# Kernel optimization log

Hardware: AMD Instinct MI355X
Metric: run time of the kernel (lower is better)

Reference implementation:

```python
import jax, jax.numpy as jnp
from jax import lax
import numpy as np

BETA = 0.5
ITERATION = 50
K = 1
EPS = 1e-5  # F.normalize eps


def cost_matrix_cosine(x, y):
    # x: [b,m,d], y: [b,n,d] -> cosine distance [b,m,n]
    xn = x / jnp.maximum(jnp.linalg.norm(x, axis=-1, keepdims=True), EPS)
    yn = y / jnp.maximum(jnp.linalg.norm(y, axis=-1, keepdims=True), EPS)
    return 1.0 - jnp.einsum('bmd,bnd->bmn', xn, yn)


def ipot(C, x_len, x_pad, y_len, y_pad, joint_pad, beta, iteration, k):
    # C: [b,m,n]; x_*: txt (m); y_*: img (n). Returns transport plan [b,m,n].
    b, m, n = C.shape
    jp_t = jnp.transpose(joint_pad, (0, 2, 1))                      # [b,n,m]
    A = jnp.where(jp_t, 0.0, jnp.exp(-jnp.transpose(C, (0, 2, 1)) / beta))
    T0 = jnp.where(jp_t, 0.0, 1.0)                                  # [b,n,m]
    sigma0 = jnp.where(x_pad, 0.0, 1.0 / x_len[:, None])[:, :, None]  # [b,m,1]
    x_mask = (x_pad.astype(C.dtype) * 1e4)[:, None, :]              # [b,1,m]
    y_mask = (y_pad.astype(C.dtype) * 1e4)[:, None, :]              # [b,1,n]
    xl = x_len[:, None, None]
    yl = y_len[:, None, None]

    def outer(carry, _):
        T, sigma = carry
        Q = A * T                                                   # [b,n,m]
        def inner(sig, _):
            # sig: [b,m,1]
            delta = 1.0 / (yl * jnp.transpose(jnp.matmul(Q, sig), (0, 2, 1)) + y_mask)  # [b,1,n]
            sig = jnp.transpose(1.0 / (xl * jnp.matmul(delta, Q) + x_mask), (0, 2, 1))  # [b,m,1]
            return sig, delta
        sigma, deltas = lax.scan(inner, sigma, None, length=k)
        delta = deltas[-1]                                          # [b,1,n]
        T = jnp.transpose(delta, (0, 2, 1)) * Q * jnp.transpose(sigma, (0, 2, 1))  # [b,n,m]
        return (T, sigma), None

    (T, _), _ = lax.scan(outer, (T0, sigma0), None, length=iteration)
    return jnp.transpose(T, (0, 2, 1))                              # [b,m,n]


def optimal_transport_dist(txt_emb, img_emb, txt_pad, img_pad):
    cost = cost_matrix_cosine(txt_emb, img_emb)                     # [b,m,n]
    joint_pad = txt_pad[:, :, None] | img_pad[:, None, :]           # [b,m,n]
    cost = jnp.where(joint_pad, 0.0, cost)
    txt_len = (txt_pad.shape[1] - jnp.sum(txt_pad, axis=1)).astype(cost.dtype)
    img_len = (img_pad.shape[1] - jnp.sum(img_pad, axis=1)).astype(cost.dtype)
    T = ipot(lax.stop_gradient(cost), txt_len, txt_pad, img_len, img_pad,
             joint_pad, BETA, ITERATION, K)
    # trace(cost @ T^T) == sum_ij cost_ij * plan_ij, per sample
    return jnp.sum(cost * lax.stop_gradient(T), axis=(1, 2))        # [b]


def reference(entitytxt_vec, object_vec, entitytxt_num, object_num):
    txt_nodes_emb = entitytxt_vec.astype(jnp.float32)               # [b,tl,d]
    img_nodes_emb = object_vec[:, 1:].astype(jnp.float32)           # [b,il,d]
    txt_pad = entitytxt_num == 0                                    # [b,tl] bool
    img_pad = object_num[:, 1:] == 0                                # [b,il] bool
    ot_dist = optimal_transport_dist(txt_nodes_emb, img_nodes_emb, txt_pad, img_pad)
    ot_loss = jnp.sum(ot_dist) * 0.01
    return ot_loss


def setup_inputs():
    key = jax.random.key(0)
    k1, k2, k3, k4 = jax.random.split(key, 4)
    b, tl, il1, d = 256, 128, 128, 1024
    entitytxt_vec = jax.random.normal(k1, (b, tl, d), dtype=jnp.float32)
    object_vec = jax.random.normal(k2, (b, il1, d), dtype=jnp.float32)
    entitytxt_num = jax.random.randint(k3, (b, tl), 0, 2, dtype=jnp.int32)
    object_num = jax.random.randint(k4, (b, il1), 0, 2, dtype=jnp.int32)
    # guarantee at least one valid node per sample (avoid 1/0 lengths)
    entitytxt_num = entitytxt_num.at[:, 0].set(1)
    object_num = object_num.at[:, 1].set(1)
    return {"entitytxt_vec": entitytxt_vec, "object_vec": object_vec,
            "entitytxt_num": entitytxt_num, "object_num": object_num}
```

## Files before the change

### kernel.cpp

```cpp
#include <hip/hip_runtime.h>
#include <math.h>

#define BATCH 256
#define M 128
#define NIMG 127
#define NP 128
#define D 1024
#define BK 64
#define NT (D / BK)
#define ITERS 50
#define LROW 72

typedef __attribute__((ext_vector_type(8))) short bf16x8;
typedef __attribute__((ext_vector_type(4))) float floatx4;

static __device__ __forceinline__ unsigned pack_bf16x2(float a, float b) {
    unsigned ua = __builtin_bit_cast(unsigned, a);
    unsigned ub = __builtin_bit_cast(unsigned, b);
    ua += 0x7fffu + ((ua >> 16) & 1u);
    ub += 0x7fffu + ((ub >> 16) & 1u);
    return (ua >> 16) | (ub & 0xffff0000u);
}

template<int CTRL>
static __device__ __forceinline__ float dpp_add(float v) {
    int s = __builtin_amdgcn_update_dpp(0, __builtin_bit_cast(int, v), CTRL, 0xf, 0xf, true);
    return v + __builtin_bit_cast(float, s);
}
static __device__ __forceinline__ float red16(float v) {
    v = dpp_add<0x121>(v);
    v = dpp_add<0x122>(v);
    v = dpp_add<0x124>(v);
    v = dpp_add<0x128>(v);
    return v;
}

static __device__ __forceinline__ void barrier_lgkm() {
    asm volatile("s_waitcnt lgkmcnt(0)" ::: "memory");
    __builtin_amdgcn_s_barrier();
    __builtin_amdgcn_sched_barrier(0);
}

static __device__ __forceinline__ void load_tile(const float* __restrict__ xb,
                                                 const float* __restrict__ yb,
                                                 int kk, int r0, int c16,
                                                 float4 (&vx)[4], float4 (&vy)[4]) {
#pragma unroll
    for (int it = 0; it < 4; ++it) {
        const int r = r0 + it * 32;
        vx[it] = *(const float4*)(xb + (size_t)r * D + kk + c16 * 4);
        float4 z = make_float4(0.f, 0.f, 0.f, 0.f);
        if (r < NIMG) z = *(const float4*)(yb + (size_t)r * D + kk + c16 * 4);
        vy[it] = z;
    }
}

static __device__ __forceinline__ void stage_tile(short* __restrict__ Xs, short* __restrict__ Ys,
                                                  int r0, int c16,
                                                  const float4 (&vx)[4], const float4 (&vy)[4],
                                                  float (&ssx)[4], float (&ssy)[4]) {
#pragma unroll
    for (int it = 0; it < 4; ++it) {
        const int r = r0 + it * 32;
        float4 v = vx[it];
        ssx[it] = fmaf(v.x, v.x, fmaf(v.y, v.y, fmaf(v.z, v.z, fmaf(v.w, v.w, ssx[it]))));
        uint2 p;
        p.x = pack_bf16x2(v.x, v.y);
        p.y = pack_bf16x2(v.z, v.w);
        *(uint2*)(&Xs[r * LROW + c16 * 4]) = p;
        v = vy[it];
        ssy[it] = fmaf(v.x, v.x, fmaf(v.y, v.y, fmaf(v.z, v.z, fmaf(v.w, v.w, ssy[it]))));
        p.x = pack_bf16x2(v.x, v.y);
        p.y = pack_bf16x2(v.z, v.w);
        *(uint2*)(&Ys[r * LROW + c16 * 4]) = p;
    }
}

static __device__ __forceinline__ void mfma_tile(const short* __restrict__ Xs,
                                                 const short* __restrict__ Ys,
                                                 int mbase, int nbase, int col, int quad,
                                                 floatx4 (&acc)[2][4]) {
#pragma unroll
    for (int ks = 0; ks < 2; ++ks) {
        const int koff = ks * 32 + quad * 8;
        bf16x8 af[2], bfr[4];
#pragma unroll
        for (int tr = 0; tr < 2; ++tr)
            af[tr] = *(const bf16x8*)(&Xs[(mbase + tr * 16 + col) * LROW + koff]);
#pragma unroll
        for (int tc = 0; tc < 4; ++tc)
            bfr[tc] = *(const bf16x8*)(&Ys[(nbase + tc * 16 + col) * LROW + koff]);
#pragma unroll
        for (int tr = 0; tr < 2; ++tr)
#pragma unroll
            for (int tc = 0; tc < 4; ++tc)
                acc[tr][tc] = __builtin_amdgcn_mfma_f32_16x16x32_bf16(
                    af[tr], bfr[tc], acc[tr][tc], 0, 0, 0);
    }
}

__launch_bounds__(512, 1)
__global__ void gemm_a_kernel(const float* __restrict__ xg,
                              const float* __restrict__ yg,
                              const int* __restrict__ xnum,
                              const int* __restrict__ ynum,
                              float* __restrict__ Aout)
{
    __shared__ __align__(16) short Xs[2][M * LROW];
    __shared__ __align__(16) short Ys[2][M * LROW];
    __shared__ __align__(16) float sinvx[M];
    __shared__ __align__(16) float sinvy[NP];
    __shared__ __align__(16) float sxmask[M];
    __shared__ __align__(16) float symask[NP];

    const int b    = blockIdx.x;
    const int t    = threadIdx.x;
    const int lane = t & 63;
    const int w    = t >> 6;

    const float* xb = xg + (size_t)b * M * D;
    const float* yb = yg + ((size_t)b * 128 + 1) * D;

    if (t < M)  sxmask[t] = (xnum[b * M + t] == 0) ? 1.0f : 0.0f;
    if (t < NP) symask[t] = (t < NIMG && ynum[b * 128 + t + 1] != 0) ? 0.0f : 1.0f;

    const int r0  = t >> 4;
    const int c16 = t & 15;

    floatx4 acc[2][4];
#pragma unroll
    for (int a = 0; a < 2; ++a)
#pragma unroll
        for (int c = 0; c < 4; ++c) acc[a][c] = (floatx4)0.0f;

    float ssx[4] = {0.f, 0.f, 0.f, 0.f};
    float ssy[4] = {0.f, 0.f, 0.f, 0.f};

    const int mbase = (w & 3) * 32;
    const int nbase = (w >> 2) * 64;
    const int col   = lane & 15;
    const int quad  = lane >> 4;

    float4 vxa[4], vya[4], vxb[4], vyb[4];
    load_tile(xb, yb, 0,  r0, c16, vxa, vya);
    load_tile(xb, yb, BK, r0, c16, vxb, vyb);

#pragma unroll 1
    for (int ii = 0; ii < NT; ii += 2) {
        stage_tile(Xs[0], Ys[0], r0, c16, vxa, vya, ssx, ssy);
        if (ii + 2 < NT) load_tile(xb, yb, (ii + 2) * BK, r0, c16, vxa, vya);
        barrier_lgkm();
        mfma_tile(Xs[0], Ys[0], mbase, nbase, col, quad, acc);
        stage_tile(Xs[1], Ys[1], r0, c16, vxb, vyb, ssx, ssy);
        if (ii + 3 < NT) load_tile(xb, yb, (ii + 3) * BK, r0, c16, vxb, vyb);
        barrier_lgkm();
        mfma_tile(Xs[1], Ys[1], mbase, nbase, col, quad, acc);
    }

#pragma unroll
    for (int it = 0; it < 4; ++it) {
        ssx[it] = red16(ssx[it]);
        ssy[it] = red16(ssy[it]);
    }
    if (c16 == 0) {
#pragma unroll
        for (int it = 0; it < 4; ++it) {
            const int r = r0 + it * 32;
            sinvx[r] = 1.0f / fmaxf(sqrtf(ssx[it]), 1e-5f);
            sinvy[r] = 1.0f / fmaxf(sqrtf(ssy[it]), 1e-5f);
        }
    }
    barrier_lgkm();

    float* Ab = Aout + (size_t)b * M * NP;
#pragma unroll
    for (int tr = 0; tr < 2; ++tr)
#pragma unroll
        for (int tc = 0; tc < 4; ++tc) {
            const int n = nbase + tc * 16 + col;
            const float ivy_n = sinvy[n];
            const float ymf   = symask[n];
#pragma unroll
            for (int reg = 0; reg < 4; ++reg) {
                const int m = mbase + tr * 16 + quad * 4 + reg;
                const float p = acc[tr][tc][reg] * sinvx[m] * ivy_n;
                const float a = (sxmask[m] + ymf > 0.0f) ? 0.0f : expf(2.0f * p - 2.0f);
                Ab[m * NP + n] = a;
            }
        }
}

__launch_bounds__(512, 1)
__global__ void ipot_kernel(const float* __restrict__ Ain,
                            const int* __restrict__ xnum,
                            const int* __restrict__ ynum,
                            float* __restrict__ out)
{
    __shared__ __align__(16) float partCS[8 * 128];
    __shared__ __align__(16) float sdelta[NP];
    __shared__ __align__(16) float sxmask[M];
    __shared__ __align__(16) float symask[NP];
    __shared__ float sxl_s, syl_s;
    __shared__ unsigned scnt[16];
    __shared__ float swsum[8];

    const int b    = blockIdx.x;
    const int t    = threadIdx.x;
    const int lane = t & 63;
    const int w    = t >> 6;
    const int tj   = t & 15;
    const int i0   = (t >> 4) * 4;
    const int j0   = tj * 8;

    bool tpad = true, ipad = true;
    if (t < M)  { tpad = (xnum[b * M + t] == 0); sxmask[t] = tpad ? 1e4f : 0.0f; }
    if (t < NP) { ipad = !(t < NIMG && ynum[b * 128 + t + 1] != 0); symask[t] = ipad ? 1e4f : 0.0f; }
    unsigned long long bx = __ballot(t < M  && !tpad);
    unsigned long long by = __ballot(t < NP && !ipad);
    if (lane == 0) { scnt[w] = (unsigned)__popcll(bx); scnt[8 + w] = (unsigned)__popcll(by); }
    __syncthreads();
    if (t == 0) {
        float xl = 0.f, yl = 0.f;
        for (int k = 0; k < 8; ++k) { xl += scnt[k]; yl += scnt[8 + k]; }
        sxl_s = xl; syl_s = yl;
    }
    __syncthreads();
    const float xl = sxl_s, yl = syl_s;

    float xm[4], ym[8];
    *(float4*)xm       = *(const float4*)(&sxmask[i0]);
    *(float4*)ym       = *(const float4*)(&symask[j0]);
    *(float4*)(ym + 4) = *(const float4*)(&symask[j0 + 4]);

    float sn[4];
#pragma unroll
    for (int r = 0; r < 4; ++r)
        sn[r] = (xm[r] > 0.0f) ? 0.0f : __builtin_amdgcn_rcpf(xl);

    const float* Ab = Ain + (size_t)b * M * NP;
    float Af[4][8], Q[4][8];
#pragma unroll
    for (int r = 0; r < 4; ++r) {
        float4 a0 = *(const float4*)(Ab + (size_t)(i0 + r) * NP + j0);
        float4 a1 = *(const float4*)(Ab + (size_t)(i0 + r) * NP + j0 + 4);
        Af[r][0] = a0.x; Af[r][1] = a0.y; Af[r][2] = a0.z; Af[r][3] = a0.w;
        Af[r][4] = a1.x; Af[r][5] = a1.y; Af[r][6] = a1.z; Af[r][7] = a1.w;
#pragma unroll
        for (int j = 0; j < 8; ++j) Q[r][j] = Af[r][j];
    }

    float lp = 0.0f;
    for (int itn = 0; itn < ITERS; ++itn) {
        float cp[8] = {0.f,0.f,0.f,0.f,0.f,0.f,0.f,0.f};
#pragma unroll
        for (int r = 0; r < 4; ++r)
#pragma unroll
            for (int j = 0; j < 8; ++j)
                cp[j] = fmaf(sn[r], Q[r][j], cp[j]);
#pragma unroll
        for (int j = 0; j < 8; ++j) {
            cp[j] += __shfl_xor(cp[j], 16);
            cp[j] += __shfl_xor(cp[j], 32);
        }
        if (lane < 16) {
            float4 c0 = make_float4(cp[0], cp[1], cp[2], cp[3]);
            float4 c1 = make_float4(cp[4], cp[5], cp[6], cp[7]);
            *(float4*)(&partCS[w * 128 + j0])     = c0;
            *(float4*)(&partCS[w * 128 + j0 + 4]) = c1;
        }
        __syncthreads();
        if (t < NP) {
            float s = 0.f;
#pragma unroll
            for (int w8 = 0; w8 < 8; ++w8) s += partCS[w8 * 128 + t];
            sdelta[t] = __builtin_amdgcn_rcpf(yl * s + symask[t]);
        }
        __syncthreads();
        float dl[8];
        *(float4*)dl       = *(const float4*)(&sdelta[j0]);
        *(float4*)(dl + 4) = *(const float4*)(&sdelta[j0 + 4]);
        float rp[4] = {0.f, 0.f, 0.f, 0.f};
#pragma unroll
        for (int r = 0; r < 4; ++r)
#pragma unroll
            for (int j = 0; j < 8; ++j)
                rp[r] = fmaf(dl[j], Q[r][j], rp[r]);
#pragma unroll
        for (int r = 0; r < 4; ++r) rp[r] = red16(rp[r]);
#pragma unroll
        for (int r = 0; r < 4; ++r) rp[r] = __shfl(rp[r], lane & 48);
#pragma unroll
        for (int r = 0; r < 4; ++r)
            sn[r] = __builtin_amdgcn_rcpf(xl * rp[r] + xm[r]);

        if (itn < ITERS - 1) {
#pragma unroll
            for (int r = 0; r < 4; ++r) {
                const float f = sn[r];
#pragma unroll
                for (int j = 0; j < 8; ++j)
                    Q[r][j] *= Af[r][j] * dl[j] * f;
            }
        } else {
#pragma unroll
            for (int r = 0; r < 4; ++r)
#pragma unroll
                for (int j = 0; j < 8; ++j) {
                    const float a = Af[r][j];
                    if (a > 0.0f)
                        lp = fmaf(-0.5f * logf(a) * dl[j] * sn[r], Q[r][j], lp);
                }
        }
    }

#pragma unroll
    for (int off = 32; off > 0; off >>= 1) lp += __shfl_down(lp, off);
    if (lane == 0) swsum[w] = lp;
    __syncthreads();
    if (t == 0) {
        float tot = 0.f;
        for (int k = 0; k < 8; ++k) tot += swsum[k];
        atomicAdd(out, 0.01f * tot);
    }
}

extern "C" void kernel_launch(void* const* d_in, const int* in_sizes, int n_in,
                              void* d_out, int out_size, void* d_ws, size_t ws_size,
                              hipStream_t stream) {
    const float* x  = (const float*)d_in[0];
    const float* y  = (const float*)d_in[1];
    const int*   xn = (const int*)d_in[2];
    const int*   yn = (const int*)d_in[3];
    float* out = (float*)d_out;
    float* A   = (float*)d_ws;

    (void)hipMemsetAsync(out, 0, (size_t)out_size * sizeof(float), stream);
    gemm_a_kernel<<<dim3(BATCH), dim3(512), 0, stream>>>(x, y, xn, yn, A);
    ipot_kernel<<<dim3(BATCH), dim3(512), 0, stream>>>(A, xn, yn, out);
}
```

Measured before the change: 346.8 us.

## Split cost GEMM over K halves and fuse normalization into IPOT kernel

Adds a GEMM kernel that splits the 1024-long reduction into two halves, launching twice as many blocks (two per batch) with launch bounds allowing two blocks per CU, and writes partial dot products and partial squared norms to workspace. A new IPOT kernel sums the partials, applies the cosine normalization and exp to build A, and keeps the iteration state in registers, updating Q in place. The aim is to fill more CUs during the GEMM phase, since 256 blocks underuse the machine. In exchange it writes and reads back twice as much intermediate data, and it falls back to the old path when the workspace is too small.

```diff
diff --git a/kernel.cpp b/kernel.cpp
--- a/kernel.cpp
+++ b/kernel.cpp
@@ -8,6 +8,8 @@
 #define D 1024
 #define BK 64
 #define NT (D / BK)
+#define KH 512
+#define NT2 (KH / BK)
 #define ITERS 50
 #define LROW 72
 
@@ -99,6 +101,244 @@
     }
 }
 
+__launch_bounds__(512, 2)
+__global__ void gemm_c_kernel(const float* __restrict__ xg,
+                              const float* __restrict__ yg,
+                              float* __restrict__ Cp,
+                              float* __restrict__ NXp,
+                              float* __restrict__ NYp)
+{
+    __shared__ __align__(16) short Xs[2][M * LROW];
+    __shared__ __align__(16) short Ys[2][M * LROW];
+
+    const int bid = blockIdx.x;
+    const int b   = bid >> 1;
+    const int kh  = bid & 1;
+    const int t   = threadIdx.x;
+    const int lane = t & 63;
+    const int w    = t >> 6;
+
+    const float* xb = xg + (size_t)b * M * D + kh * KH;
+    const float* yb = yg + ((size_t)b * 128 + 1) * D + kh * KH;
+
+    const int r0  = t >> 4;
+    const int c16 = t & 15;
+
+    floatx4 acc[2][4];
+#pragma unroll
+    for (int a = 0; a < 2; ++a)
+#pragma unroll
+        for (int c = 0; c < 4; ++c) acc[a][c] = (floatx4)0.0f;
+
+    float ssx[4] = {0.f, 0.f, 0.f, 0.f};
+    float ssy[4] = {0.f, 0.f, 0.f, 0.f};
+
+    const int mbase = (w & 3) * 32;
+    const int nbase = (w >> 2) * 64;
+    const int col   = lane & 15;
+    const int quad  = lane >> 4;
+
+    float4 vxa[4], vya[4], vxb[4], vyb[4];
+    load_tile(xb, yb, 0,  r0, c16, vxa, vya);
+    load_tile(xb, yb, BK, r0, c16, vxb, vyb);
+
+#pragma unroll 1
+    for (int ii = 0; ii < NT2; ii += 2) {
+        stage_tile(Xs[0], Ys[0], r0, c16, vxa, vya, ssx, ssy);
+        if (ii + 2 < NT2) load_tile(xb, yb, (ii + 2) * BK, r0, c16, vxa, vya);
+        barrier_lgkm();
+        mfma_tile(Xs[0], Ys[0], mbase, nbase, col, quad, acc);
+        stage_tile(Xs[1], Ys[1], r0, c16, vxb, vyb, ssx, ssy);
+        if (ii + 3 < NT2) load_tile(xb, yb, (ii + 3) * BK, r0, c16, vxb, vyb);
+        barrier_lgkm();
+        mfma_tile(Xs[1], Ys[1], mbase, nbase, col, quad, acc);
+    }
+
+#pragma unroll
+    for (int it = 0; it < 4; ++it) {
+        ssx[it] = red16(ssx[it]);
+        ssy[it] = red16(ssy[it]);
+    }
+    if (c16 == 0) {
+#pragma unroll
+        for (int it = 0; it < 4; ++it) {
+            const int r = r0 + it * 32;
+            NXp[(size_t)bid * M + r] = ssx[it];
+            NYp[(size_t)bid * M + r] = ssy[it];
+        }
+    }
+
+    float* Cb = Cp + (size_t)bid * M * NP;
+#pragma unroll
+    for (int tr = 0; tr < 2; ++tr)
+#pragma unroll
+        for (int tc = 0; tc < 4; ++tc) {
+            const int n = nbase + tc * 16 + col;
+#pragma unroll
+            for (int reg = 0; reg < 4; ++reg) {
+                const int m = mbase + tr * 16 + quad * 4 + reg;
+                Cb[m * NP + n] = acc[tr][tc][reg];
+            }
+        }
+}
+
+__launch_bounds__(512, 1)
+__global__ void ipot_fused_kernel(const float* __restrict__ Cp,
+                                  const float* __restrict__ NXp,
+                                  const float* __restrict__ NYp,
+                                  const int* __restrict__ xnum,
+                                  const int* __restrict__ ynum,
+                                  float* __restrict__ out)
+{
+    __shared__ __align__(16) float partCS[8 * 128];
+    __shared__ __align__(16) float sdelta[NP];
+    __shared__ __align__(16) float sxmask[M];
+    __shared__ __align__(16) float symask[NP];
+    __shared__ __align__(16) float sinvx[M];
+    __shared__ __align__(16) float sinvy[NP];
+    __shared__ float sxl_s, syl_s;
+    __shared__ unsigned scnt[16];
+    __shared__ float swsum[8];
+
+    const int b    = blockIdx.x;
+    const int t    = threadIdx.x;
+    const int lane = t & 63;
+    const int w    = t >> 6;
+    const int tj   = t & 15;
+    const int i0   = (t >> 4) * 4;
+    const int j0   = tj * 8;
+
+    bool tpad = true, ipad = true;
+    if (t < M)  { tpad = (xnum[b * M + t] == 0); sxmask[t] = tpad ? 1e4f : 0.0f; }
+    if (t < NP) { ipad = !(t < NIMG && ynum[b * 128 + t + 1] != 0); symask[t] = ipad ? 1e4f : 0.0f; }
+    if (t < M) {
+        const float q = NXp[(size_t)(2 * b) * M + t] + NXp[(size_t)(2 * b + 1) * M + t];
+        sinvx[t] = 1.0f / fmaxf(sqrtf(q), 1e-5f);
+    }
+    if (t < NP) {
+        const float q = NYp[(size_t)(2 * b) * M + t] + NYp[(size_t)(2 * b + 1) * M + t];
+        sinvy[t] = 1.0f / fmaxf(sqrtf(q), 1e-5f);
+    }
+    unsigned long long bx = __ballot(t < M  && !tpad);
+    unsigned long long by = __ballot(t < NP && !ipad);
+    if (lane == 0) { scnt[w] = (unsigned)__popcll(bx); scnt[8 + w] = (unsigned)__popcll(by); }
+    __syncthreads();
+    if (t == 0) {
+        float xl = 0.f, yl = 0.f;
+        for (int k = 0; k < 8; ++k) { xl += scnt[k]; yl += scnt[8 + k]; }
+        sxl_s = xl; syl_s = yl;
+    }
+    __syncthreads();
+    const float xl = sxl_s, yl = syl_s;
+
+    float xm[4], ym[8], ivx[4], ivy[8];
+    *(float4*)xm       = *(const float4*)(&sxmask[i0]);
+    *(float4*)ym       = *(const float4*)(&symask[j0]);
+    *(float4*)(ym + 4) = *(const float4*)(&symask[j0 + 4]);
+    *(float4*)ivx       = *(const float4*)(&sinvx[i0]);
+    *(float4*)ivy       = *(const float4*)(&sinvy[j0]);
+    *(float4*)(ivy + 4) = *(const float4*)(&sinvy[j0 + 4]);
+
+    float sn[4];
+#pragma unroll
+    for (int r = 0; r < 4; ++r)
+        sn[r] = (xm[r] > 0.0f) ? 0.0f : __builtin_amdgcn_rcpf(xl);
+
+    const float* C0 = Cp + (size_t)(2 * b) * M * NP;
+    const float* C1 = Cp + (size_t)(2 * b + 1) * M * NP;
+    float Af[4][8], Q[4][8];
+#pragma unroll
+    for (int r = 0; r < 4; ++r) {
+        float4 a0 = *(const float4*)(C0 + (size_t)(i0 + r) * NP + j0);
+        float4 a1 = *(const float4*)(C0 + (size_t)(i0 + r) * NP + j0 + 4);
+        float4 b0 = *(const float4*)(C1 + (size_t)(i0 + r) * NP + j0);
+        float4 b1 = *(const float4*)(C1 + (size_t)(i0 + r) * NP + j0 + 4);
+        float c[8] = {a0.x + b0.x, a0.y + b0.y, a0.z + b0.z, a0.w + b0.w,
+                      a1.x + b1.x, a1.y + b1.y, a1.z + b1.z, a1.w + b1.w};
+#pragma unroll
+        for (int j = 0; j < 8; ++j) {
+            const bool pad = (xm[r] > 0.0f) || (ym[j] > 0.0f);
+            const float p  = c[j] * ivx[r] * ivy[j];
+            Af[r][j] = pad ? 0.0f : expf(2.0f * p - 2.0f);
+            Q[r][j]  = Af[r][j];
+        }
+    }
+
+    float lp = 0.0f;
+    for (int itn = 0; itn < ITERS; ++itn) {
+        float cp[8] = {0.f,0.f,0.f,0.f,0.f,0.f,0.f,0.f};
+#pragma unroll
+        for (int r = 0; r < 4; ++r)
+#pragma unroll
+            for (int j = 0; j < 8; ++j)
+                cp[j] = fmaf(sn[r], Q[r][j], cp[j]);
+#pragma unroll
+        for (int j = 0; j < 8; ++j) {
+            cp[j] += __shfl_xor(cp[j], 16);
+            cp[j] += __shfl_xor(cp[j], 32);
+        }
+        if (lane < 16) {
+            float4 c0 = make_float4(cp[0], cp[1], cp[2], cp[3]);
+            float4 c1 = make_float4(cp[4], cp[5], cp[6], cp[7]);
+            *(float4*)(&partCS[w * 128 + j0])     = c0;
+            *(float4*)(&partCS[w * 128 + j0 + 4]) = c1;
+        }
+        __syncthreads();
+        if (t < NP) {
+            float s = 0.f;
+#pragma unroll
+            for (int w8 = 0; w8 < 8; ++w8) s += partCS[w8 * 128 + t];
+            sdelta[t] = __builtin_amdgcn_rcpf(yl * s + symask[t]);
+        }
+        __syncthreads();
+        float dl[8];
+        *(float4*)dl       = *(const float4*)(&sdelta[j0]);
+        *(float4*)(dl + 4) = *(const float4*)(&sdelta[j0 + 4]);
+        float rp[4] = {0.f, 0.f, 0.f, 0.f};
+#pragma unroll
+        for (int r = 0; r < 4; ++r)
+#pragma unroll
+            for (int j = 0; j < 8; ++j)
+                rp[r] = fmaf(dl[j], Q[r][j], rp[r]);
+#pragma unroll
+        for (int r = 0; r < 4; ++r) rp[r] = red16(rp[r]);
+#pragma unroll
+        for (int r = 0; r < 4; ++r) rp[r] = __shfl(rp[r], lane & 48);
+#pragma unroll
+        for (int r = 0; r < 4; ++r)
+            sn[r] = __builtin_amdgcn_rcpf(xl * rp[r] + xm[r]);
+
+        if (itn < ITERS - 1) {
+#pragma unroll
+            for (int r = 0; r < 4; ++r) {
+                const float f = sn[r];
+#pragma unroll
+                for (int j = 0; j < 8; ++j)
+                    Q[r][j] *= Af[r][j] * dl[j] * f;
+            }
+        } else {
+#pragma unroll
+            for (int r = 0; r < 4; ++r)
+#pragma unroll
+                for (int j = 0; j < 8; ++j) {
+                    const float a = Af[r][j];
+                    if (a > 0.0f)
+                        lp = fmaf(-0.5f * logf(a) * dl[j] * sn[r], Q[r][j], lp);
+                }
+        }
+    }
+
+#pragma unroll
+    for (int off = 32; off > 0; off >>= 1) lp += __shfl_down(lp, off);
+    if (lane == 0) swsum[w] = lp;
+    __syncthreads();
+    if (t == 0) {
+        float tot = 0.f;
+        for (int k = 0; k < 8; ++k) tot += swsum[k];
+        atomicAdd(out, 0.01f * tot);
+    }
+}
+
 __launch_bounds__(512, 1)
 __global__ void gemm_a_kernel(const float* __restrict__ xg,
                               const float* __restrict__ yg,
@@ -332,9 +572,22 @@
     const int*   xn = (const int*)d_in[2];
     const int*   yn = (const int*)d_in[3];
     float* out = (float*)d_out;
-    float* A   = (float*)d_ws;
 
     (void)hipMemsetAsync(out, 0, (size_t)out_size * sizeof(float), stream);
-    gemm_a_kernel<<<dim3(BATCH), dim3(512), 0, stream>>>(x, y, xn, yn, A);
-    ipot_kernel<<<dim3(BATCH), dim3(512), 0, stream>>>(A, xn, yn, out);
-}
+
+    const size_t cpFloats = (size_t)2 * BATCH * M * NP;
+    const size_t nFloats  = (size_t)2 * BATCH * M;
+    const size_t needBytes = (cpFloats + 2 * nFloats) * sizeof(float);
+
+    if (ws_size >= needBytes) {
+        float* Cp  = (float*)d_ws;
+        float* NXp = Cp + cpFloats;
+        float* NYp = NXp + nFloats;
+        gemm_c_kernel<<<dim3(2 * BATCH), dim3(512), 0, stream>>>(x, y, Cp, NXp, NYp);
+        ipot_fused_kernel<<<dim3(BATCH), dim3(512), 0, stream>>>(Cp, NXp, NYp, xn, yn, out);
+    } else {
+        float* A = (float*)d_ws;
+        gemm_a_kernel<<<dim3(BATCH), dim3(512), 0, stream>>>(x, y, xn, yn, A);
+        ipot_kernel<<<dim3(BATCH), dim3(512), 0, stream>>>(A, xn, yn, out);
+    }
+}
```

Measured after the change: 347.9 us. Within noise of the previous version (+0.3%).

## Fuse cosine-GEMM and IPOT kernels, keep A matrix in shared memory

Applied to the files above, without the earlier changes.

Merges the GEMM/exp kernel and the IPOT iteration kernel into a single per-batch kernel. The A matrix is written to LDS, reusing the staging buffers with a padded stride, rather than being round-tripped through global workspace. This removes one kernel launch and the global write and read of A. In exchange, the IPOT phase now runs in the same workgroup after the GEMM, so the two phases can no longer overlap across kernels, and LDS aliasing needs correct barriers.

```diff
diff --git a/kernel.cpp b/kernel.cpp
--- a/kernel.cpp
+++ b/kernel.cpp
@@ -10,6 +10,7 @@
 #define NT (D / BK)
 #define ITERS 50
 #define LROW 72
+#define ASTRIDE 132
 
 typedef __attribute__((ext_vector_type(8))) short bf16x8;
 typedef __attribute__((ext_vector_type(4))) float floatx4;
@@ -100,109 +101,26 @@
 }
 
 __launch_bounds__(512, 1)
-__global__ void gemm_a_kernel(const float* __restrict__ xg,
-                              const float* __restrict__ yg,
-                              const int* __restrict__ xnum,
-                              const int* __restrict__ ynum,
-                              float* __restrict__ Aout)
+__global__ void fused_kernel(const float* __restrict__ xg,
+                             const float* __restrict__ yg,
+                             const int* __restrict__ xnum,
+                             const int* __restrict__ ynum,
+                             float* __restrict__ out)
 {
-    __shared__ __align__(16) short Xs[2][M * LROW];
-    __shared__ __align__(16) short Ys[2][M * LROW];
-    __shared__ __align__(16) float sinvx[M];
-    __shared__ __align__(16) float sinvy[NP];
-    __shared__ __align__(16) float sxmask[M];
-    __shared__ __align__(16) float symask[NP];
-
-    const int b    = blockIdx.x;
-    const int t    = threadIdx.x;
-    const int lane = t & 63;
-    const int w    = t >> 6;
-
-    const float* xb = xg + (size_t)b * M * D;
-    const float* yb = yg + ((size_t)b * 128 + 1) * D;
-
-    if (t < M)  sxmask[t] = (xnum[b * M + t] == 0) ? 1.0f : 0.0f;
-    if (t < NP) symask[t] = (t < NIMG && ynum[b * 128 + t + 1] != 0) ? 0.0f : 1.0f;
-
-    const int r0  = t >> 4;
-    const int c16 = t & 15;
-
-    floatx4 acc[2][4];
-#pragma unroll
-    for (int a = 0; a < 2; ++a)
-#pragma unroll
-        for (int c = 0; c < 4; ++c) acc[a][c] = (floatx4)0.0f;
-
-    float ssx[4] = {0.f, 0.f, 0.f, 0.f};
-    float ssy[4] = {0.f, 0.f, 0.f, 0.f};
-
-    const int mbase = (w & 3) * 32;
-    const int nbase = (w >> 2) * 64;
-    const int col   = lane & 15;
-    const int quad  = lane >> 4;
-
-    float4 vxa[4], vya[4], vxb[4], vyb[4];
-    load_tile(xb, yb, 0,  r0, c16, vxa, vya);
-    load_tile(xb, yb, BK, r0, c16, vxb, vyb);
-
-#pragma unroll 1
-    for (int ii = 0; ii < NT; ii += 2) {
-        stage_tile(Xs[0], Ys[0], r0, c16, vxa, vya, ssx, ssy);
-        if (ii + 2 < NT) load_tile(xb, yb, (ii + 2) * BK, r0, c16, vxa, vya);
-        barrier_lgkm();
-        mfma_tile(Xs[0], Ys[0], mbase, nbase, col, quad, acc);
-        stage_tile(Xs[1], Ys[1], r0, c16, vxb, vyb, ssx, ssy);
-        if (ii + 3 < NT) load_tile(xb, yb, (ii + 3) * BK, r0, c16, vxb, vyb);
-        barrier_lgkm();
-        mfma_tile(Xs[1], Ys[1], mbase, nbase, col, quad, acc);
-    }
-
-#pragma unroll
-    for (int it = 0; it < 4; ++it) {
-        ssx[it] = red16(ssx[it]);
-        ssy[it] = red16(ssy[it]);
-    }
-    if (c16 == 0) {
-#pragma unroll
-        for (int it = 0; it < 4; ++it) {
-            const int r = r0 + it * 32;
-            sinvx[r] = 1.0f / fmaxf(sqrtf(ssx[it]), 1e-5f);
-            sinvy[r] = 1.0f / fmaxf(sqrtf(ssy[it]), 1e-5f);
-        }
-    }
-    barrier_lgkm();
-
-    float* Ab = Aout + (size_t)b * M * NP;
-#pragma unroll
-    for (int tr = 0; tr < 2; ++tr)
-#pragma unroll
-        for (int tc = 0; tc < 4; ++tc) {
-            const int n = nbase + tc * 16 + col;
-            const float ivy_n = sinvy[n];
-            const float ymf   = symask[n];
-#pragma unroll
-            for (int reg = 0; reg < 4; ++reg) {
-                const int m = mbase + tr * 16 + quad * 4 + reg;
-                const float p = acc[tr][tc][reg] * sinvx[m] * ivy_n;
-                const float a = (sxmask[m] + ymf > 0.0f) ? 0.0f : expf(2.0f * p - 2.0f);
-                Ab[m * NP + n] = a;
-            }
-        }
-}
-
-__launch_bounds__(512, 1)
-__global__ void ipot_kernel(const float* __restrict__ Ain,
-                            const int* __restrict__ xnum,
-                            const int* __restrict__ ynum,
-                            float* __restrict__ out)
-{
+    __shared__ __align__(16) unsigned char smem[2 * M * LROW * 2 * sizeof(short)];
     __shared__ __align__(16) float partCS[8 * 128];
     __shared__ __align__(16) float sdelta[NP];
     __shared__ __align__(16) float sxmask[M];
     __shared__ __align__(16) float symask[NP];
+    __shared__ __align__(16) float sinvx[M];
+    __shared__ __align__(16) float sinvy[NP];
     __shared__ float sxl_s, syl_s;
     __shared__ unsigned scnt[16];
     __shared__ float swsum[8];
+
+    short (*Xs)[M * LROW] = reinterpret_cast<short (*)[M * LROW]>(smem);
+    short (*Ys)[M * LROW] = reinterpret_cast<short (*)[M * LROW]>(smem + 2 * M * LROW * sizeof(short));
+    float* Alds = reinterpret_cast<float*>(smem);
 
     const int b    = blockIdx.x;
     const int t    = threadIdx.x;
@@ -224,7 +142,76 @@
         for (int k = 0; k < 8; ++k) { xl += scnt[k]; yl += scnt[8 + k]; }
         sxl_s = xl; syl_s = yl;
     }
+
+    const float* xb = xg + (size_t)b * M * D;
+    const float* yb = yg + ((size_t)b * 128 + 1) * D;
+
+    const int r0  = t >> 4;
+    const int c16 = t & 15;
+
+    floatx4 acc[2][4];
+#pragma unroll
+    for (int a = 0; a < 2; ++a)
+#pragma unroll
+        for (int c = 0; c < 4; ++c) acc[a][c] = (floatx4)0.0f;
+
+    float ssx[4] = {0.f, 0.f, 0.f, 0.f};
+    float ssy[4] = {0.f, 0.f, 0.f, 0.f};
+
+    const int mbase = (w & 3) * 32;
+    const int nbase = (w >> 2) * 64;
+    const int col   = lane & 15;
+    const int quad  = lane >> 4;
+
+    float4 vxa[4], vya[4], vxb[4], vyb[4];
+    load_tile(xb, yb, 0,  r0, c16, vxa, vya);
+    load_tile(xb, yb, BK, r0, c16, vxb, vyb);
     __syncthreads();
+
+#pragma unroll 1
+    for (int ii = 0; ii < NT; ii += 2) {
+        stage_tile(Xs[0], Ys[0], r0, c16, vxa, vya, ssx, ssy);
+        if (ii + 2 < NT) load_tile(xb, yb, (ii + 2) * BK, r0, c16, vxa, vya);
+        barrier_lgkm();
+        mfma_tile(Xs[0], Ys[0], mbase, nbase, col, quad, acc);
+        stage_tile(Xs[1], Ys[1], r0, c16, vxb, vyb, ssx, ssy);
+        if (ii + 3 < NT) load_tile(xb, yb, (ii + 3) * BK, r0, c16, vxb, vyb);
+        barrier_lgkm();
+        mfma_tile(Xs[1], Ys[1], mbase, nbase, col, quad, acc);
+    }
+
+#pragma unroll
+    for (int it = 0; it < 4; ++it) {
+        ssx[it] = red16(ssx[it]);
+        ssy[it] = red16(ssy[it]);
+    }
+    if (c16 == 0) {
+#pragma unroll
+        for (int it = 0; it < 4; ++it) {
+            const int r = r0 + it * 32;
+            sinvx[r] = 1.0f / fmaxf(sqrtf(ssx[it]), 1e-5f);
+            sinvy[r] = 1.0f / fmaxf(sqrtf(ssy[it]), 1e-5f);
+        }
+    }
+    barrier_lgkm();
+
+#pragma unroll
+    for (int tr = 0; tr < 2; ++tr)
+#pragma unroll
+        for (int tc = 0; tc < 4; ++tc) {
+            const int n = nbase + tc * 16 + col;
+            const float ivy_n = sinvy[n];
+            const float ymf   = symask[n];
+#pragma unroll
+            for (int reg = 0; reg < 4; ++reg) {
+                const int m = mbase + tr * 16 + quad * 4 + reg;
+                const float p = acc[tr][tc][reg] * sinvx[m] * ivy_n;
+                const float a = (sxmask[m] + ymf > 0.0f) ? 0.0f : expf(2.0f * p - 2.0f);
+                Alds[m * ASTRIDE + n] = a;
+            }
+        }
+    barrier_lgkm();
+
     const float xl = sxl_s, yl = syl_s;
 
     float xm[4], ym[8];
@@ -237,17 +224,17 @@
     for (int r = 0; r < 4; ++r)
         sn[r] = (xm[r] > 0.0f) ? 0.0f : __builtin_amdgcn_rcpf(xl);
 
-    const float* Ab = Ain + (size_t)b * M * NP;
     float Af[4][8], Q[4][8];
 #pragma unroll
     for (int r = 0; r < 4; ++r) {
-        float4 a0 = *(const float4*)(Ab + (size_t)(i0 + r) * NP + j0);
-        float4 a1 = *(const float4*)(Ab + (size_t)(i0 + r) * NP + j0 + 4);
+        float4 a0 = *(const float4*)(&Alds[(i0 + r) * ASTRIDE + j0]);
+        float4 a1 = *(const float4*)(&Alds[(i0 + r) * ASTRIDE + j0 + 4]);
         Af[r][0] = a0.x; Af[r][1] = a0.y; Af[r][2] = a0.z; Af[r][3] = a0.w;
         Af[r][4] = a1.x; Af[r][5] = a1.y; Af[r][6] = a1.z; Af[r][7] = a1.w;
 #pragma unroll
         for (int j = 0; j < 8; ++j) Q[r][j] = Af[r][j];
     }
+    __syncthreads();
 
     float lp = 0.0f;
     for (int itn = 0; itn < ITERS; ++itn) {
@@ -332,9 +319,8 @@
     const int*   xn = (const int*)d_in[2];
     const int*   yn = (const int*)d_in[3];
     float* out = (float*)d_out;
-    float* A   = (float*)d_ws;
+    (void)d_ws; (void)ws_size;
 
     (void)hipMemsetAsync(out, 0, (size_t)out_size * sizeof(float), stream);
-    gemm_a_kernel<<<dim3(BATCH), dim3(512), 0, stream>>>(x, y, xn, yn, A);
-    ipot_kernel<<<dim3(BATCH), dim3(512), 0, stream>>>(A, xn, yn, out);
-}
+    fused_kernel<<<dim3(BATCH), dim3(512), 0, stream>>>(x, y, xn, yn, out);
+}
```

Measured after the change: 343.6 us. Within noise of the previous version (-0.9%).
